# Optimization experiments

Measured on AMD Instinct MI355X. Metric: run time of the kernel, lower is better.

Reference implementation:

```python
import jax, jax.numpy as jnp
import numpy as np

B, F, H, W_, N = 1, 256, 64, 64, 25

def setup_inputs() -> dict:
    key = jax.random.key(0)
    k1, k2 = jax.random.split(key)
    image_embedding = jax.random.normal(k1, (B, F, H, W_, N), dtype=jnp.float32)
    # Per-channel neighborhood weights, initialized like the torch module:
    # 1e-4 everywhere, 1.0 at the center slice, then perturbed so grads are non-trivial.
    base = jnp.full((F, N), 1e-4, dtype=jnp.float32).at[:, N // 2].set(1.0)
    W = base + 0.01 * jax.random.normal(k2, (F, N), dtype=jnp.float32)
    return {"image_embedding": image_embedding, "W": W}

def reference(image_embedding, W):
    # Fused equivalent of 256 per-channel Linear(N->1, bias=False) launches:
    # compressed[b,f,h,w] = sum_n image_embedding[b,f,h,w,n] * W[f,n]
    compressed = jnp.einsum('bfhwn,fn->bfhw', image_embedding, W)
    return compressed
```

## Files before the change

kernel.cpp:

```cpp
#include <hip/hip_runtime.h>


constexpr int NN    = 25;
constexpr int BLOCK = 256;
constexpr int WAVES = BLOCK / 64;
constexpr int OPW   = 64;
constexpr int FPW   = OPW * NN;

typedef __attribute__((address_space(3))) void       lds_void;
typedef const __attribute__((address_space(1))) void gbl_void;

__global__ __launch_bounds__(BLOCK) void medsam_compress_kernel(
    const float* __restrict__ img,
    const float* __restrict__ W,
    float* __restrict__ out)
{
    __shared__ float lds[WAVES][FPW];

    const int tid  = threadIdx.x;
    const int w    = tid >> 6;
    const int lane = tid & 63;
    const int gw   = blockIdx.x * WAVES + w;

    const float* gbase = img + (long long)gw * FPW;

    #pragma unroll
    for (int k = 0; k < 6; ++k) {
        __builtin_amdgcn_global_load_lds(
            (gbl_void*)(gbase + k * 256 + lane * 4),
            (lds_void*)&lds[w][k * 256],
            16, 0, 0);
    }
    __builtin_amdgcn_global_load_lds(
        (gbl_void*)(gbase + 1536 + lane),
        (lds_void*)&lds[w][1536],
        4, 0, 0);

    const int f = __builtin_amdgcn_readfirstlane(gw >> 6);
    const float* __restrict__ Wf = W + f * NN;
    float wreg[NN];
    #pragma unroll
    for (int n = 0; n < NN; ++n) wreg[n] = Wf[n];

    asm volatile("s_waitcnt vmcnt(0)" ::: "memory");
    __builtin_amdgcn_sched_barrier(0);

    const float* row = &lds[w][lane * NN];
    float acc = 0.f;
    #pragma unroll
    for (int n = 0; n < NN; ++n)
        acc += row[n] * wreg[n];

    out[(long long)gw * OPW + lane] = acc;
}

extern "C" void kernel_launch(void* const* d_in, const int* in_sizes, int n_in,
                              void* d_out, int out_size, void* d_ws, size_t ws_size,
                              hipStream_t stream) {
    const float* img = (const float*)d_in[0];
    const float* W   = (const float*)d_in[1];
    float* out       = (float*)d_out;

    const int grid = out_size / (OPW * WAVES);
    medsam_compress_kernel<<<grid, BLOCK, 0, stream>>>(img, W, out);
}
```

Baseline: 21.26 us.

## Make kernel persistent with double-buffered LDS prefetch of next chunk

Replaces the one-chunk-per-wave launch with a fixed grid of persistent blocks where each wave loops over chunks, prefetching the next chunk into a second LDS buffer via global_load_lds while computing the current one. It aims to overlap memory fetch with the dot-product compute and cut launch and wave startup overhead. It doubles the LDS footprint per wave, which lowers occupancy, and relies on vmcnt counting to order the loads.

Result: no change. 21.34 us (+0.4%).

```diff
diff --git a/kernel.cpp b/kernel.cpp
--- a/kernel.cpp
+++ b/kernel.cpp
@@ -3,55 +3,73 @@
 
 constexpr int NN    = 25;
 constexpr int BLOCK = 256;
-constexpr int WAVES = BLOCK / 64;
+constexpr int WAVES = 4;
 constexpr int OPW   = 64;
 constexpr int FPW   = OPW * NN;
+constexpr int GRID  = 768;
 
 typedef __attribute__((address_space(3))) void       lds_void;
 typedef const __attribute__((address_space(1))) void gbl_void;
 
+__device__ __forceinline__ void stage_chunk(float* lds_dst, const float* gsrc,
+                                            int lane) {
+    #pragma unroll
+    for (int k = 0; k < 6; ++k)
+        __builtin_amdgcn_global_load_lds(
+            (gbl_void*)(gsrc + k * 256 + lane * 4),
+            (lds_void*)(lds_dst + k * 256), 16, 0, 0);
+    __builtin_amdgcn_global_load_lds(
+        (gbl_void*)(gsrc + 1536 + lane),
+        (lds_void*)(lds_dst + 1536), 4, 0, 0);
+}
+
 __global__ __launch_bounds__(BLOCK) void medsam_compress_kernel(
     const float* __restrict__ img,
     const float* __restrict__ W,
-    float* __restrict__ out)
+    float* __restrict__ out,
+    int nchunk)
 {
-    __shared__ float lds[WAVES][FPW];
+    __shared__ float lds[WAVES][2][FPW];
 
     const int tid  = threadIdx.x;
     const int w    = tid >> 6;
     const int lane = tid & 63;
-    const int gw   = blockIdx.x * WAVES + w;
+    const int gw0  = __builtin_amdgcn_readfirstlane(blockIdx.x * WAVES + w);
+    const int step = GRID * WAVES;
 
-    const float* gbase = img + (long long)gw * FPW;
+    int c   = gw0;
+    int cur = 0;
 
-    #pragma unroll
-    for (int k = 0; k < 6; ++k) {
-        __builtin_amdgcn_global_load_lds(
-            (gbl_void*)(gbase + k * 256 + lane * 4),
-            (lds_void*)&lds[w][k * 256],
-            16, 0, 0);
+    if (c < nchunk)
+        stage_chunk(&lds[w][0][0], img + (long long)c * FPW, lane);
+
+    while (c < nchunk) {
+        const int nxt = c + step;
+        if (nxt < nchunk) {
+            stage_chunk(&lds[w][cur ^ 1][0], img + (long long)nxt * FPW, lane);
+            asm volatile("s_waitcnt vmcnt(7)" ::: "memory");
+        } else {
+            asm volatile("s_waitcnt vmcnt(0)" ::: "memory");
+        }
+        __builtin_amdgcn_sched_barrier(0);
+
+        const int f = c >> 6;
+        const float* __restrict__ Wf = W + f * NN;
+        float wreg[NN];
+        #pragma unroll
+        for (int n = 0; n < NN; ++n) wreg[n] = Wf[n];
+
+        const float* row = &lds[w][cur][lane * NN];
+        float acc = 0.f;
+        #pragma unroll
+        for (int n = 0; n < NN; ++n)
+            acc += row[n] * wreg[n];
+
+        out[(long long)c * OPW + lane] = acc;
+
+        cur ^= 1;
+        c = nxt;
     }
-    __builtin_amdgcn_global_load_lds(
-        (gbl_void*)(gbase + 1536 + lane),
-        (lds_void*)&lds[w][1536],
-        4, 0, 0);
-
-    const int f = __builtin_amdgcn_readfirstlane(gw >> 6);
-    const float* __restrict__ Wf = W + f * NN;
-    float wreg[NN];
-    #pragma unroll
-    for (int n = 0; n < NN; ++n) wreg[n] = Wf[n];
-
-    asm volatile("s_waitcnt vmcnt(0)" ::: "memory");
-    __builtin_amdgcn_sched_barrier(0);
-
-    const float* row = &lds[w][lane * NN];
-    float acc = 0.f;
-    #pragma unroll
-    for (int n = 0; n < NN; ++n)
-        acc += row[n] * wreg[n];
-
-    out[(long long)gw * OPW + lane] = acc;
 }
 
 extern "C" void kernel_launch(void* const* d_in, const int* in_sizes, int n_in,
@@ -61,6 +79,6 @@
     const float* W   = (const float*)d_in[1];
     float* out       = (float*)d_out;
 
-    const int grid = out_size / (OPW * WAVES);
-    medsam_compress_kernel<<<grid, BLOCK, 0, stream>>>(img, W, out);
+    const int nchunk = out_size / OPW;
+    medsam_compress_kernel<<<GRID, BLOCK, 0, stream>>>(img, W, out, nchunk);
 }
```
